# Performance work log

Hardware: AMD Instinct MI355X
Metric: run time of the kernel (lower is better)

## Reference

```python
import jax, jax.numpy as jnp
import numpy as np

B, C_IN, NF, H, W, L = 8, 64, 64, 96, 96, 13
NEG_SLOPE = 0.2


def conv2d(x, w, b, pad):
    # x: [B,C,H,W], w: [O,I,kh,kw]
    y = jax.lax.conv_general_dilated(
        x, w, window_strides=(1, 1), padding=[(pad, pad), (pad, pad)],
        dimension_numbers=("NCHW", "OIHW", "NCHW"))
    return y + b[None, :, None, None]


def leaky(x):
    return jax.nn.leaky_relu(x, NEG_SLOPE)


def bilinear_sample(img, px, py):
    # img: [B,C,H,W]; px,py: [B,H,W] pixel coords; zero padding outside.
    Bs, C, Hs, Ws = img.shape
    x0 = jnp.floor(px)
    y0 = jnp.floor(py)
    wx = px - x0
    wy = py - y0
    x0i = x0.astype(jnp.int32)
    y0i = y0.astype(jnp.int32)
    imgf = img.reshape(Bs, C, Hs * Ws)

    def gather(xi, yi):
        valid = ((xi >= 0) & (xi < Ws) & (yi >= 0) & (yi < Hs)).astype(img.dtype)
        xc = jnp.clip(xi, 0, Ws - 1)
        yc = jnp.clip(yi, 0, Hs - 1)
        idx = (yc * Ws + xc).reshape(Bs, 1, Hs * Ws)
        v = jnp.take_along_axis(imgf, idx, axis=2).reshape(Bs, C, Hs, Ws)
        return v * valid[:, None, :, :]

    return (gather(x0i, y0i) * ((1 - wx) * (1 - wy))[:, None]
            + gather(x0i + 1, y0i) * (wx * (1 - wy))[:, None]
            + gather(x0i, y0i + 1) * ((1 - wx) * wy)[:, None]
            + gather(x0i + 1, y0i + 1) * (wx * wy)[:, None])


def warp(img, flow):
    # img: [B,C,H,W]; flow: [B,2,H,W] (dx=flow[:,0], dy=flow[:,1])
    Bs, C, Hs, Ws = img.shape
    xx = jnp.arange(Ws, dtype=img.dtype)[None, None, :]  # [1,1,W]
    yy = jnp.arange(Hs, dtype=img.dtype)[None, :, None]  # [1,H,1]
    vx = xx + flow[:, 0]  # [B,H,W]
    vy = yy + flow[:, 1]
    # torch grid_sample(align_corners=False) with normalization 2*v/(dim-1)-1:
    # sample pixel = v*dim/(dim-1) - 0.5
    px = vx * (Ws / (Ws - 1)) - 0.5
    py = vy * (Hs / (Hs - 1)) - 0.5
    return bilinear_sample(img, px, py)


def setup_inputs() -> dict:
    key = jax.random.key(0)
    ks = jax.random.split(key, 13)
    s = 0.05
    return {
        "x": jax.random.normal(ks[0], (B, C_IN, H, W), jnp.float32),
        "m": jax.random.normal(ks[1], (B, NF, H, W), jnp.float32),
        "prev_h": jax.random.normal(ks[2], (B, NF, H, W), jnp.float32),
        "w_i2h": jax.random.normal(ks[3], (3 * NF, C_IN, 3, 3), jnp.float32) * s,
        "b_i2h": jnp.zeros((3 * NF,), jnp.float32),
        "w_i2f": jax.random.normal(ks[4], (32, C_IN, 5, 5), jnp.float32) * s,
        "b_i2f": jnp.zeros((32,), jnp.float32),
        "w_h2f": jax.random.normal(ks[5], (32, NF, 5, 5), jnp.float32) * s,
        "b_h2f": jnp.zeros((32,), jnp.float32),
        "w_fl": jax.random.normal(ks[6], (2 * L, 32, 5, 5), jnp.float32) * s,
        "b_fl": jnp.zeros((2 * L,), jnp.float32),
        "w_ret": jax.random.normal(ks[7], (3 * NF, NF * L, 1, 1), jnp.float32) * s,
        "b_ret": jnp.zeros((3 * NF,), jnp.float32),
    }


def reference(x, m, prev_h, w_i2h, b_i2h, w_i2f, b_i2f, w_h2f, b_h2f, w_fl, b_fl, w_ret, b_ret):
    # input-to-hidden gates
    i2h = conv2d(x, w_i2h, b_i2h, pad=1)              # [B,3NF,H,W]
    i0, i1, i2 = jnp.split(i2h, 3, axis=1)
    # flow generator
    f = leaky(conv2d(x, w_i2f, b_i2f, pad=2) + conv2d(prev_h, w_h2f, b_h2f, pad=2))
    flows = conv2d(f, w_fl, b_fl, pad=2)              # [B,2L,H,W]
    flows = flows.reshape(B, L, 2, H, W)
    # warp prev_h by -flow for each link (vectorized over L)
    warped = jax.vmap(lambda fl: warp(prev_h, -fl), in_axes=1, out_axes=1)(flows)
    warped = warped.reshape(B, L * NF, H, W)
    h2h = conv2d(warped, w_ret, b_ret, pad=0)         # [B,3NF,H,W]
    h0, h1, h2 = jnp.split(h2h, 3, axis=1)
    reset_gate = jax.nn.sigmoid(i0 + h0)
    update_gate = jax.nn.sigmoid(i1 + h1)
    new_mem = leaky(i2 + reset_gate * h2)
    next_h = update_gate * prev_h + (1.0 - update_gate) * new_mem
    return (next_h, m, next_h)
```

## Files before the change

kernel.cpp:

```cpp
#include <hip/hip_runtime.h>
#include <hip/hip_bf16.h>
#include <hip/hip_fp16.h>

typedef unsigned short u16;
typedef unsigned int u32;
typedef __attribute__((ext_vector_type(8))) _Float16 f16x8;
typedef __attribute__((ext_vector_type(4))) float f32x4;

#define NEG 0.2f

__device__ __forceinline__ float bf2f(u16 u) {
    return __uint_as_float(((u32)u) << 16);
}
__device__ __forceinline__ u16 f2b(float f) {
    u32 u = __float_as_uint(f);
    u32 r = (u + 0x7FFF + ((u >> 16) & 1)) >> 16;
    return (u16)r;
}
__device__ __forceinline__ u16 f2h(float f) {
    return __half_as_ushort(__float2half(f));
}
__device__ __forceinline__ float h2f(u16 u) {
    return __half2float(__ushort_as_half(u));
}
__device__ __forceinline__ float sigm(float x) {
    return 1.0f / (1.0f + __expf(-x));
}
__device__ __forceinline__ float ldin(const void* p, int idx, int flag) {
    if (flag) return ((const float*)p)[idx];
    return bf2f(((const u16*)p)[idx]);
}
__device__ __forceinline__ u16 ldin_h(const void* p, int idx, int flag) {
    if (flag) return f2h(((const float*)p)[idx]);
    return f2h(bf2f(((const u16*)p)[idx]));
}


#define WS_NEED 60371008u

__global__ void kdetect(const u16* __restrict__ x, u32* __restrict__ flag)
{
    __shared__ u32 mx[256];
    int t = threadIdx.x;
    u32 m = 0;
    for (int i = t; i < 8192; i += 256) {
        u32 e = ((u32)x[i] >> 7) & 0xFF;
        m = m > e ? m : e;
    }
    mx[t] = m;
    __syncthreads();
    for (int s = 128; s > 0; s >>= 1) {
        if (t < s) mx[t] = mx[t] > mx[t + s] ? mx[t] : mx[t + s];
        __syncthreads();
    }
    if (t == 0) flag[0] = (mx[0] > 0xC0) ? 1u : 0u;
}

__global__ void kprep(const void* __restrict__ w_i2h, const void* __restrict__ w_i2f,
                      const void* __restrict__ w_h2f, const void* __restrict__ w_fl,
                      const void* __restrict__ w_ret,
                      const void* __restrict__ b_i2h, const void* __restrict__ b_i2f,
                      const void* __restrict__ b_h2f, const void* __restrict__ b_fl,
                      const void* __restrict__ b_ret,
                      u16* __restrict__ wiA, u16* __restrict__ wfA,
                      u16* __restrict__ wlA, u16* __restrict__ wretA,
                      float* __restrict__ biases, const u32* __restrict__ flag)
{
    int flg = (int)flag[0];
    int i = blockIdx.x * 256 + threadIdx.x;
    if (i < 110592) {
        int j = i & 7; int lane = (i >> 3) & 63; int rest = i >> 9;
        int cib = rest & 1; int rest2 = rest >> 1;
        int tap = rest2 % 9; int mt = rest2 / 9;
        int oc = mt * 16 + (lane & 15);
        int ci = cib * 32 + ((lane >> 4) << 3) + j;
        wiA[i] = ldin_h(w_i2h, (oc * 64 + ci) * 9 + tap, flg);
    }
    if (i < 102400) {
        int j = i & 7; int lane = (i >> 3) & 63; int rest = i >> 9;
        int cib = rest & 3; int rest2 = rest >> 2;
        int tap = rest2 % 25; int mt = rest2 / 25;
        int oc = mt * 16 + (lane & 15);
        int cip = cib * 32 + ((lane >> 4) << 3) + j;
        wfA[i] = (cip < 64) ? ldin_h(w_i2f, (oc * 64 + cip) * 25 + tap, flg)
                            : ldin_h(w_h2f, (oc * 64 + cip - 64) * 25 + tap, flg);
    }
    if (i < 25600) {
        int j = i & 7; int lane = (i >> 3) & 63; int rest = i >> 9;
        int tap = rest % 25; int mt = rest / 25;
        int oc = mt * 16 + (lane & 15);
        int ci = ((lane >> 4) << 3) + j;
        wlA[i] = (oc < 26) ? ldin_h(w_fl, (oc * 32 + ci) * 25 + tap, flg) : (u16)0;
    }
    if (i < 159744) {
        int j = i & 7; int l = (i >> 3) & 63; int rest = i >> 9;
        int ks = rest % 26; int mt = rest / 26;
        int o = mt * 16 + (l & 15);
        int k = ks * 32 + ((l >> 4) << 3) + j;
        wretA[i] = ldin_h(w_ret, o * 832 + k, flg);
    }
    if (i < 474) {
        float v;
        if (i < 192)      v = ldin(b_i2h, i, flg);
        else if (i < 224) v = ldin(b_i2f, i - 192, flg);
        else if (i < 256) v = ldin(b_h2f, i - 224, flg);
        else if (i < 282) v = ldin(b_fl, i - 256, flg);
        else              v = ldin(b_ret, i - 282, flg);
        biases[i] = v;
    }
}

__global__ __launch_bounds__(256) void kxph(const void* __restrict__ x,
        const void* __restrict__ ph, u16* __restrict__ xph,
        const u32* __restrict__ flag)
{
    __shared__ __align__(16) u16 tile[64 * 104];
    int flg = (int)flag[0];
    int h = blockIdx.x, b = blockIdx.y;
    int t = threadIdx.x;
#pragma unroll 1
    for (int s = 0; s < 2; s++) {
        const void* src = s ? ph : x;
#pragma unroll 1
        for (int i = t; i < 768; i += 256) {
            int wc = i % 12, c = i / 12;
            int base = ((b * 64 + c) * 96 + h) * 96 + wc * 8;
            u16 r[8];
            if (flg) {
                const float* sp = (const float*)src + base;
                float4 f0 = *(const float4*)sp;
                float4 f1 = *(const float4*)(sp + 4);
                r[0] = f2h(f0.x); r[1] = f2h(f0.y); r[2] = f2h(f0.z); r[3] = f2h(f0.w);
                r[4] = f2h(f1.x); r[5] = f2h(f1.y); r[6] = f2h(f1.z); r[7] = f2h(f1.w);
            } else {
                const u16* sp = (const u16*)src + base;
                uint4 u = *(const uint4*)sp;
                r[0] = f2h(bf2f((u16)(u.x & 0xFFFF))); r[1] = f2h(bf2f((u16)(u.x >> 16)));
                r[2] = f2h(bf2f((u16)(u.y & 0xFFFF))); r[3] = f2h(bf2f((u16)(u.y >> 16)));
                r[4] = f2h(bf2f((u16)(u.z & 0xFFFF))); r[5] = f2h(bf2f((u16)(u.z >> 16)));
                r[6] = f2h(bf2f((u16)(u.w & 0xFFFF))); r[7] = f2h(bf2f((u16)(u.w >> 16)));
            }
            uint4 o;
            o.x = r[0] | ((u32)r[1] << 16); o.y = r[2] | ((u32)r[3] << 16);
            o.z = r[4] | ((u32)r[5] << 16); o.w = r[6] | ((u32)r[7] << 16);
            *(uint4*)&tile[c * 104 + wc * 8] = o;
        }
        __syncthreads();
#pragma unroll 1
        for (int i = t; i < 768; i += 256) {
            int cg = i & 7, w = i >> 3;
            u16 v[8];
#pragma unroll
            for (int k = 0; k < 8; k++) v[k] = tile[(cg * 8 + k) * 104 + w];
            uint4 o;
            o.x = v[0] | ((u32)v[1] << 16); o.y = v[2] | ((u32)v[3] << 16);
            o.z = v[4] | ((u32)v[5] << 16); o.w = v[6] | ((u32)v[7] << 16);
            *(uint4*)&xph[(((b * 96 + h) * 96 + w) << 7) + s * 64 + cg * 8] = o;
        }
        __syncthreads();
    }
}

__global__ __launch_bounds__(256) void k_i2h(const u16* __restrict__ xph,
        const u16* __restrict__ wiA, const float* __restrict__ biases,
        u16* __restrict__ i2hT)
{
    __shared__ __align__(16) u16 xl[3 * 98 * 72];
    int lin = blockIdx.x;
    int b = lin & 7;
    int h = lin >> 3;
    int t = threadIdx.x, lane = t & 63, wv = t >> 6;
    int n = lane & 15, quad = lane >> 4;

#pragma unroll 1
    for (int i = t; i < 2352; i += 256) {
        int co = i & 7; int pos = i >> 3; int xx = pos % 98; int yy = pos / 98;
        int gy = h + yy - 1, gx = xx - 1;
        uint4 v = make_uint4(0, 0, 0, 0);
        if (gy >= 0 && gy < 96 && gx >= 0 && gx < 96)
            v = *(const uint4*)&xph[((((b * 96 + gy) * 96 + gx)) << 7) + (co << 3)];
        *(uint4*)&xl[(yy * 98 + xx) * 72 + (co << 3)] = v;
    }
    __syncthreads();

    int mt0 = wv * 3;
    f32x4 acc[3][6] = {};
    const f16x8* A = (const f16x8*)wiA;
    f16x8 aC[3], aN[3];
#pragma unroll
    for (int mi = 0; mi < 3; mi++)
        aC[mi] = A[(((mt0 + mi) * 9 + 0) * 2 + 0) * 64 + lane];
#pragma unroll 1
    for (int it = 0; it < 18; it++) {
        int tap = it >> 1, cib = it & 1;
        if (it < 17) {
            int tn = it + 1; int tapn = tn >> 1, cibn = tn & 1;
#pragma unroll
            for (int mi = 0; mi < 3; mi++)
                aN[mi] = A[(((mt0 + mi) * 9 + tapn) * 2 + cibn) * 64 + lane];
        }
        int dy = tap / 3, dx = tap % 3;
        __builtin_amdgcn_s_setprio(1);
#pragma unroll
        for (int g = 0; g < 6; g++) {
            f16x8 bb = *(const f16x8*)&xl[(dy * 98 + g * 16 + n + dx) * 72 + cib * 32 + quad * 8];
#pragma unroll
            for (int mi = 0; mi < 3; mi++)
                acc[mi][g] = __builtin_amdgcn_mfma_f32_16x16x32_f16(aC[mi], bb, acc[mi][g], 0, 0, 0);
        }
        __builtin_amdgcn_s_setprio(0);
#pragma unroll
        for (int mi = 0; mi < 3; mi++) aC[mi] = aN[mi];
    }

#pragma unroll
    for (int mi = 0; mi < 3; mi++) {
        int ocb = (mt0 + mi) * 16 + quad * 4;
        float b0 = biases[ocb + 0], b1 = biases[ocb + 1];
        float b2 = biases[ocb + 2], b3 = biases[ocb + 3];
#pragma unroll
        for (int g = 0; g < 6; g++) {
            u16 p0 = f2h(acc[mi][g][0] + b0);
            u16 p1 = f2h(acc[mi][g][1] + b1);
            u16 p2 = f2h(acc[mi][g][2] + b2);
            u16 p3 = f2h(acc[mi][g][3] + b3);
            int base = (((b * 96 + h) * 96 + g * 16 + n)) * 192 + ocb;
            *(uint2*)&i2hT[base] =
                make_uint2(p0 | ((u32)p1 << 16), p2 | ((u32)p3 << 16));
        }
    }
}

__global__ __launch_bounds__(256) void k_flowfeat(const u16* __restrict__ xph,
        const u16* __restrict__ wfA, const float* __restrict__ biases,
        u16* __restrict__ fT)
{
    __shared__ __align__(16) u16 xl[8 * 20 * 136];
    int lin = blockIdx.x;
    int b = lin & 7;
    int r = lin >> 3;
    int x0 = (r % 6) * 16, y0 = (r / 6) * 4;
    int t = threadIdx.x, lane = t & 63, wv = t >> 6;
    int n = lane & 15, quad = lane >> 4;

    for (int i = t; i < 2560; i += 256) {
        int co = i & 15; int pos = i >> 4; int xx = pos % 20; int yy = pos / 20;
        int gy = y0 + yy - 2, gx = x0 + xx - 2;
        uint4 v = make_uint4(0, 0, 0, 0);
        if (gy >= 0 && gy < 96 && gx >= 0 && gx < 96)
            v = *(const uint4*)&xph[((((b * 96 + gy) * 96 + gx)) << 7) + (co << 3)];
        *(uint4*)&xl[(yy * 20 + xx) * 136 + (co << 3)] = v;
    }
    __syncthreads();

    f32x4 acc0 = {}, acc1 = {};
    const f16x8* A = (const f16x8*)wfA;
    f16x8 bbC[4], a0C[4], a1C[4];
    {
        int rowb = (wv * 20 + n) * 136 + quad * 8;
#pragma unroll
        for (int cib = 0; cib < 4; cib++) {
            bbC[cib] = *(const f16x8*)&xl[rowb + cib * 32];
            a0C[cib] = A[cib * 64 + lane];
            a1C[cib] = A[(100 + cib) * 64 + lane];
        }
    }
#pragma unroll 1
    for (int tap = 0; tap < 25; tap++) {
        f16x8 bbN[4], a0N[4], a1N[4];
        if (tap < 24) {
            int tn = tap + 1;
            int dy = tn / 5, dx = tn % 5;
            int rowb = ((wv + dy) * 20 + n + dx) * 136 + quad * 8;
#pragma unroll
            for (int cib = 0; cib < 4; cib++) {
                bbN[cib] = *(const f16x8*)&xl[rowb + cib * 32];
                a0N[cib] = A[(tn * 4 + cib) * 64 + lane];
                a1N[cib] = A[((25 + tn) * 4 + cib) * 64 + lane];
            }
        }
#pragma unroll
        for (int cib = 0; cib < 4; cib++) {
            acc0 = __builtin_amdgcn_mfma_f32_16x16x32_f16(a0C[cib], bbC[cib], acc0, 0, 0, 0);
            acc1 = __builtin_amdgcn_mfma_f32_16x16x32_f16(a1C[cib], bbC[cib], acc1, 0, 0, 0);
        }
#pragma unroll
        for (int cib = 0; cib < 4; cib++) {
            bbC[cib] = bbN[cib]; a0C[cib] = a0N[cib]; a1C[cib] = a1N[cib];
        }
    }

    int base = (((b * 96 + y0 + wv) * 96 + x0 + n)) * 32 + quad * 4;
    {
        u16 p[4];
#pragma unroll
        for (int r2 = 0; r2 < 4; r2++) {
            int oc = quad * 4 + r2;
            float v = acc0[r2] + biases[192 + oc] + biases[224 + oc];
            v = (v > 0.f) ? v : NEG * v;
            p[r2] = f2h(v);
        }
        *(uint2*)&fT[base] = make_uint2(p[0] | ((u32)p[1] << 16), p[2] | ((u32)p[3] << 16));
#pragma unroll
        for (int r2 = 0; r2 < 4; r2++) {
            int oc = 16 + quad * 4 + r2;
            float v = acc1[r2] + biases[192 + oc] + biases[224 + oc];
            v = (v > 0.f) ? v : NEG * v;
            p[r2] = f2h(v);
        }
        *(uint2*)&fT[base + 16] = make_uint2(p[0] | ((u32)p[1] << 16), p[2] | ((u32)p[3] << 16));
    }
}

__global__ __launch_bounds__(256) void k_flows(const u16* __restrict__ fT,
        const u16* __restrict__ wlA, const float* __restrict__ biases,
        float* __restrict__ flows)
{
    __shared__ __align__(16) u16 xl[8 * 20 * 40];
    int lin = blockIdx.x;
    int b = lin & 7;
    int r = lin >> 3;
    int x0 = (r % 6) * 16, y0 = (r / 6) * 4;
    int t = threadIdx.x, lane = t & 63, wv = t >> 6;
    int n = lane & 15, quad = lane >> 4;

    for (int i = t; i < 640; i += 256) {
        int co = i & 3; int pos = i >> 2; int xx = pos % 20; int yy = pos / 20;
        int gy = y0 + yy - 2, gx = x0 + xx - 2;
        uint4 v = make_uint4(0, 0, 0, 0);
        if (gy >= 0 && gy < 96 && gx >= 0 && gx < 96)
            v = *(const uint4*)&fT[((((b * 96 + gy) * 96 + gx)) << 5) + (co << 3)];
        *(uint4*)&xl[(yy * 20 + xx) * 40 + (co << 3)] = v;
    }
    __syncthreads();

    f32x4 acc0 = {}, acc1 = {};
    const f16x8* A = (const f16x8*)wlA;
#pragma unroll 5
    for (int tap = 0; tap < 25; tap++) {
        int dy = tap / 5, dx = tap % 5;
        f16x8 bb = *(const f16x8*)&xl[((wv + dy) * 20 + n + dx) * 40 + quad * 8];
        f16x8 a0 = A[tap * 64 + lane];
        f16x8 a1 = A[(25 + tap) * 64 + lane];
        acc0 = __builtin_amdgcn_mfma_f32_16x16x32_f16(a0, bb, acc0, 0, 0, 0);
        acc1 = __builtin_amdgcn_mfma_f32_16x16x32_f16(a1, bb, acc1, 0, 0, 0);
    }

    int pix = (y0 + wv) * 96 + x0 + n;
#pragma unroll
    for (int r2 = 0; r2 < 4; r2++) {
        int oc = quad * 4 + r2;
        flows[(b * 26 + oc) * 9216 + pix] = acc0[r2] + biases[256 + oc];
        int oc1 = 16 + quad * 4 + r2;
        if (oc1 < 26)
            flows[(b * 26 + oc1) * 9216 + pix] = acc1[r2] + biases[256 + oc1];
    }
}

__global__ __launch_bounds__(256, 4) void k_fused(const float* __restrict__ flows,
        const u16* __restrict__ xph, const u16* __restrict__ i2hT,
        const u16* __restrict__ wretA, const float* __restrict__ biases,
        void* __restrict__ out, const u32* __restrict__ flag)
{
    __shared__ __align__(16) u16 gb[2][32][72];
    __shared__ __align__(16) float hh[192 * 33];

    int flg = (int)flag[0];
    int lin = blockIdx.x;
    int b = lin & 7;
    int r = lin >> 3;
    int w0 = (r % 3) * 32;
    int h = r / 3;
    int t = threadIdx.x;
    int lane = t & 63, wv = t >> 6;
    const float S = 96.f / 95.f;
    int hrow = h * 96 + w0;

    int p = t >> 3, sub = t & 7;
    const float* fl = &flows[b * 26 * 9216 + hrow + p];
    const u16* xb = &xph[(b * 96) * 96 * 128 + 64 + sub * 8];

    int n = lane & 15, q = lane >> 4;
    int mt0 = wv * 3;
    f32x4 acc[3][2] = {};
    const f16x8* Ap = (const f16x8*)wretA;
    const f16x8 zv = {};

    f16x8 c00, c10, c01, c11; float cwx, cwy;
    f16x8 n00, n10, n01, n11; float nwx, nwy;
    float fdxc, fdyc, fdxn, fdyn;

#define GISSUE(DX, DY, V00, V10, V01, V11, WX, WY)                         \
    {                                                                      \
        float px = ((float)(w0 + p) - (DX)) * S - 0.5f;                    \
        float py = ((float)h - (DY)) * S - 0.5f;                           \
        float fx = floorf(px), fy = floorf(py);                            \
        int ix = (int)fx, iy = (int)fy;                                    \
        WX = px - fx; WY = py - fy;                                        \
        bool xv0 = (ix >= 0) & (ix < 96);                                  \
        bool xv1 = (ix >= -1) & (ix < 95);                                 \
        bool yv0 = (iy >= 0) & (iy < 96);                                  \
        bool yv1 = (iy >= -1) & (iy < 95);                                 \
        V00 = zv; V10 = zv; V01 = zv; V11 = zv;                            \
        if (yv0) {                                                         \
            const u16* rr = xb + (iy * 96 + ix) * 128;                     \
            if (xv0) V00 = *(const f16x8*)rr;                              \
            if (xv1) V10 = *(const f16x8*)(rr + 128);                      \
        }                                                                  \
        if (yv1) {                                                         \
            const u16* rr = xb + ((iy + 1) * 96 + ix) * 128;               \
            if (xv0) V01 = *(const f16x8*)rr;                              \
            if (xv1) V11 = *(const f16x8*)(rr + 128);                      \
        }                                                                  \
    }

    fdxc = fl[0 * 9216]; fdyc = fl[1 * 9216];
    fdxn = fl[2 * 9216]; fdyn = fl[3 * 9216];
    GISSUE(fdxc, fdyc, c00, c10, c01, c11, cwx, cwy);

#pragma unroll
    for (int l = 0; l < 13; l++) {
        float fdx2 = 0.f, fdy2 = 0.f;
        if (l + 2 < 13) { fdx2 = fl[(2 * l + 4) * 9216]; fdy2 = fl[(2 * l + 5) * 9216]; }
        if (l + 1 < 13) GISSUE(fdxn, fdyn, n00, n10, n01, n11, nwx, nwy);
        {
            float w00 = (1.f - cwx) * (1.f - cwy), w10 = cwx * (1.f - cwy);
            float w01 = (1.f - cwx) * cwy,         w11 = cwx * cwy;
            u16 res[8];
#pragma unroll
            for (int j = 0; j < 8; j++) {
                float v = w00 * (float)c00[j] + w10 * (float)c10[j]
                        + w01 * (float)c01[j] + w11 * (float)c11[j];
                res[j] = f2h(v);
            }
            uint4 o;
            o.x = res[0] | ((u32)res[1] << 16); o.y = res[2] | ((u32)res[3] << 16);
            o.z = res[4] | ((u32)res[5] << 16); o.w = res[6] | ((u32)res[7] << 16);
            *(uint4*)&gb[l & 1][p][sub * 8] = o;
        }
        __syncthreads();
        __builtin_amdgcn_s_setprio(1);
#pragma unroll
        for (int ksl = 0; ksl < 2; ksl++) {
            int ks = 2 * l + ksl;
            f16x8 b0 = *(const f16x8*)&gb[l & 1][n][ksl * 32 + q * 8];
            f16x8 b1 = *(const f16x8*)&gb[l & 1][16 + n][ksl * 32 + q * 8];
#pragma unroll
            for (int mi = 0; mi < 3; mi++) {
                f16x8 a = Ap[((mt0 + mi) * 26 + ks) * 64 + lane];
                acc[mi][0] = __builtin_amdgcn_mfma_f32_16x16x32_f16(a, b0, acc[mi][0], 0, 0, 0);
                acc[mi][1] = __builtin_amdgcn_mfma_f32_16x16x32_f16(a, b1, acc[mi][1], 0, 0, 0);
            }
        }
        __builtin_amdgcn_s_setprio(0);
        c00 = n00; c10 = n10; c01 = n01; c11 = n11; cwx = nwx; cwy = nwy;
        fdxc = fdxn; fdyc = fdyn; fdxn = fdx2; fdyn = fdy2;
    }
#undef GISSUE

#pragma unroll
    for (int mi = 0; mi < 3; mi++) {
        int ob = (mt0 + mi) * 16 + q * 4;
#pragma unroll
        for (int ni = 0; ni < 2; ni++)
#pragma unroll
            for (int r2 = 0; r2 < 4; r2++) {
                int o = ob + r2;
                hh[o * 33 + ni * 16 + n] = acc[mi][ni][r2] + biases[282 + o];
            }
    }
    __syncthreads();

#pragma unroll 1
    for (int j = 0; j < 8; j++) {
        int i = t + 256 * j;
        int cc = i & 63, pp = i >> 6;
        float h0v = hh[cc * 33 + pp];
        float h1v = hh[(64 + cc) * 33 + pp];
        float h2v = hh[(128 + cc) * 33 + pp];
        int pix = (b * 96 + h) * 96 + w0 + pp;
        float i0 = h2f(i2hT[pix * 192 + cc]);
        float i1 = h2f(i2hT[pix * 192 + 64 + cc]);
        float i2 = h2f(i2hT[pix * 192 + 128 + cc]);
        float pv = h2f(xph[(pix << 7) + 64 + cc]);
        float rg = sigm(i0 + h0v);
        float ug = sigm(i1 + h1v);
        float nm = i2 + rg * h2v;
        nm = (nm > 0.f) ? nm : NEG * nm;
        float nh = ug * pv + (1.f - ug) * nm;
        hh[cc * 33 + pp] = nh;
    }
    __syncthreads();

#pragma unroll 1
    for (int j = 0; j < 8; j++) {
        int i = t + 256 * j;
        int pp = i & 31, cc = i >> 5;
        float nh = hh[cc * 33 + pp];
        int oidx = ((b * 64 + cc) * 96 + h) * 96 + w0 + pp;
        if (flg) {
            float* of = (float*)out;
            of[oidx] = nh;
            of[oidx + 2 * 4718592] = nh;
        } else {
            u16* ob16 = (u16*)out;
            u16 v = f2b(nh);
            ob16[oidx] = v;
            ob16[oidx + 2 * 4718592] = v;
        }
    }
}

__global__ void kcopym(const uint4* __restrict__ m, uint4* __restrict__ out,
                       const u32* __restrict__ flag)
{
    int flg = (int)flag[0];
    int n4 = flg ? 1179648 : 589824;
    int stride = gridDim.x * 256;
    for (int i = blockIdx.x * 256 + threadIdx.x; i < n4; i += stride)
        out[n4 + i] = m[i];
}

extern "C" void kernel_launch(void* const* d_in, const int* in_sizes, int n_in,
                              void* d_out, int out_size, void* d_ws, size_t ws_size,
                              hipStream_t stream)
{
    const void* x     = d_in[0];
    const void* m     = d_in[1];
    const void* ph    = d_in[2];
    const void* w_i2h = d_in[3];
    const void* b_i2h = d_in[4];
    const void* w_i2f = d_in[5];
    const void* b_i2f = d_in[6];
    const void* w_h2f = d_in[7];
    const void* b_h2f = d_in[8];
    const void* w_fl  = d_in[9];
    const void* b_fl  = d_in[10];
    const void* w_ret = d_in[11];
    const void* b_ret = d_in[12];

    char* ws = (char*)d_ws;
    u32*    flag   = (u32*)  (ws + 0);
    u16*    wiA    = (u16*)  (ws + 64);
    u16*    wfA    = (u16*)  (ws + 221248);
    u16*    wlA    = (u16*)  (ws + 426048);
    u16*    wretA  = (u16*)  (ws + 477248);
    float*  biases = (float*)(ws + 796736);
    u16*    xph    = (u16*)  (ws + 798784);
    u16*    i2hT   = (u16*)  (ws + 19673152);
    u16*    fT     = (u16*)  (ws + 47984704);
    float*  flows  = (float*)(ws + 52703296);
    if (ws_size < WS_NEED) return;

    kdetect<<<1, 256, 0, stream>>>((const u16*)x, flag);
    kprep<<<624, 256, 0, stream>>>(w_i2h, w_i2f, w_h2f, w_fl, w_ret,
                                   b_i2h, b_i2f, b_h2f, b_fl, b_ret,
                                   wiA, wfA, wlA, wretA, biases, flag);
    kxph<<<dim3(96, 8), 256, 0, stream>>>(x, ph, xph, flag);
    k_i2h<<<dim3(768), 256, 0, stream>>>(xph, wiA, biases, i2hT);
    k_flowfeat<<<dim3(1152), 256, 0, stream>>>(xph, wfA, biases, fT);
    k_flows<<<dim3(1152), 256, 0, stream>>>(fT, wlA, biases, flows);
    k_fused<<<dim3(2304), 256, 0, stream>>>(flows, xph, i2hT, wretA, biases,
                                            d_out, flag);
    kcopym<<<2048, 256, 0, stream>>>((const uint4*)m, (uint4*)d_out, flag);
}
```

Before: 293.0 us.

## Fuse i2h convolution into the fused warp/GRU kernel and drop the i2hT buffer

Removes the separate k_i2h kernel and computes the 3x3 input-to-hidden convolution inside k_fused, staging a 3-row x tile with an XOR-swizzled layout in shared memory. The output-channel-to-wave mapping changes to wv+4*mi so that each thread holds matching i0/i1/i2 and h0/h1/h2 values, which lets the GRU gate math run directly on registers instead of through a 192-channel shared-memory staging pass. This cuts the i2hT global write and read traffic and one kernel launch, and shrinks shared memory. In exchange, k_fused gains more registers and extra prologue work while launch bounds ask for 4 blocks per CU.

```diff
diff --git a/kernel.cpp b/kernel.cpp
--- a/kernel.cpp
+++ b/kernel.cpp
@@ -161,76 +161,6 @@
     }
 }
 
-__global__ __launch_bounds__(256) void k_i2h(const u16* __restrict__ xph,
-        const u16* __restrict__ wiA, const float* __restrict__ biases,
-        u16* __restrict__ i2hT)
-{
-    __shared__ __align__(16) u16 xl[3 * 98 * 72];
-    int lin = blockIdx.x;
-    int b = lin & 7;
-    int h = lin >> 3;
-    int t = threadIdx.x, lane = t & 63, wv = t >> 6;
-    int n = lane & 15, quad = lane >> 4;
-
-#pragma unroll 1
-    for (int i = t; i < 2352; i += 256) {
-        int co = i & 7; int pos = i >> 3; int xx = pos % 98; int yy = pos / 98;
-        int gy = h + yy - 1, gx = xx - 1;
-        uint4 v = make_uint4(0, 0, 0, 0);
-        if (gy >= 0 && gy < 96 && gx >= 0 && gx < 96)
-            v = *(const uint4*)&xph[((((b * 96 + gy) * 96 + gx)) << 7) + (co << 3)];
-        *(uint4*)&xl[(yy * 98 + xx) * 72 + (co << 3)] = v;
-    }
-    __syncthreads();
-
-    int mt0 = wv * 3;
-    f32x4 acc[3][6] = {};
-    const f16x8* A = (const f16x8*)wiA;
-    f16x8 aC[3], aN[3];
-#pragma unroll
-    for (int mi = 0; mi < 3; mi++)
-        aC[mi] = A[(((mt0 + mi) * 9 + 0) * 2 + 0) * 64 + lane];
-#pragma unroll 1
-    for (int it = 0; it < 18; it++) {
-        int tap = it >> 1, cib = it & 1;
-        if (it < 17) {
-            int tn = it + 1; int tapn = tn >> 1, cibn = tn & 1;
-#pragma unroll
-            for (int mi = 0; mi < 3; mi++)
-                aN[mi] = A[(((mt0 + mi) * 9 + tapn) * 2 + cibn) * 64 + lane];
-        }
-        int dy = tap / 3, dx = tap % 3;
-        __builtin_amdgcn_s_setprio(1);
-#pragma unroll
-        for (int g = 0; g < 6; g++) {
-            f16x8 bb = *(const f16x8*)&xl[(dy * 98 + g * 16 + n + dx) * 72 + cib * 32 + quad * 8];
-#pragma unroll
-            for (int mi = 0; mi < 3; mi++)
-                acc[mi][g] = __builtin_amdgcn_mfma_f32_16x16x32_f16(aC[mi], bb, acc[mi][g], 0, 0, 0);
-        }
-        __builtin_amdgcn_s_setprio(0);
-#pragma unroll
-        for (int mi = 0; mi < 3; mi++) aC[mi] = aN[mi];
-    }
-
-#pragma unroll
-    for (int mi = 0; mi < 3; mi++) {
-        int ocb = (mt0 + mi) * 16 + quad * 4;
-        float b0 = biases[ocb + 0], b1 = biases[ocb + 1];
-        float b2 = biases[ocb + 2], b3 = biases[ocb + 3];
-#pragma unroll
-        for (int g = 0; g < 6; g++) {
-            u16 p0 = f2h(acc[mi][g][0] + b0);
-            u16 p1 = f2h(acc[mi][g][1] + b1);
-            u16 p2 = f2h(acc[mi][g][2] + b2);
-            u16 p3 = f2h(acc[mi][g][3] + b3);
-            int base = (((b * 96 + h) * 96 + g * 16 + n)) * 192 + ocb;
-            *(uint2*)&i2hT[base] =
-                make_uint2(p0 | ((u32)p1 << 16), p2 | ((u32)p3 << 16));
-        }
-    }
-}
-
 __global__ __launch_bounds__(256) void k_flowfeat(const u16* __restrict__ xph,
         const u16* __restrict__ wfA, const float* __restrict__ biases,
         u16* __restrict__ fT)
@@ -358,12 +288,15 @@
 }
 
 __global__ __launch_bounds__(256, 4) void k_fused(const float* __restrict__ flows,
-        const u16* __restrict__ xph, const u16* __restrict__ i2hT,
+        const u16* __restrict__ xph, const u16* __restrict__ wiA,
         const u16* __restrict__ wretA, const float* __restrict__ biases,
         void* __restrict__ out, const u32* __restrict__ flag)
 {
-    __shared__ __align__(16) u16 gb[2][32][72];
-    __shared__ __align__(16) float hh[192 * 33];
+    __shared__ __align__(16) char sm[26368];
+    u16* xi  = (u16*)sm;
+    u16* pvs = (u16*)(sm + 13056);
+    u16 (*gb)[32][72] = (u16 (*)[32][72])(sm + 17152);
+    float* wst = (float*)(sm + 17152);
 
     int flg = (int)flag[0];
     int lin = blockIdx.x;
@@ -376,27 +309,78 @@
     const float S = 96.f / 95.f;
     int hrow = h * 96 + w0;
 
+#pragma unroll 1
+    for (int i = t; i < 816; i += 256) {
+        int co = i & 7; int pos = i >> 3;
+        int px = pos % 34, dy = pos / 34;
+        int gy = h + dy - 1, gx = w0 + px - 1;
+        uint4 v = make_uint4(0, 0, 0, 0);
+        if (gy >= 0 && gy < 96 && gx >= 0 && gx < 96)
+            v = *(const uint4*)&xph[(((b * 96 + gy) * 96 + gx) << 7) + (co << 3)];
+        *(uint4*)&xi[((dy * 34 + px) << 6) + ((co ^ (px & 7)) << 3)] = v;
+    }
+    {
+        int co = t & 7; int px = t >> 3;
+        uint4 v = *(const uint4*)&xph[(((b * 96 + h) * 96 + w0 + px) << 7) + 64 + (co << 3)];
+        *(uint4*)&pvs[(px << 6) + ((co ^ (px & 7)) << 3)] = v;
+    }
+    __syncthreads();
+
     int p = t >> 3, sub = t & 7;
     const float* fl = &flows[b * 26 * 9216 + hrow + p];
     const u16* xb = &xph[(b * 96) * 96 * 128 + 64 + sub * 8];
 
     int n = lane & 15, q = lane >> 4;
-    int mt0 = wv * 3;
+    const f16x8* Ap = (const f16x8*)wretA;
+    const f16x8* Ai = (const f16x8*)wiA;
+    const f16x8 zv = {};
+
+    float fdxc = fl[0 * 9216], fdyc = fl[1 * 9216];
+    float fdxn = fl[2 * 9216], fdyn = fl[3 * 9216];
+
+    f32x4 acc2[3][2] = {};
+    {
+        f16x8 aC[3], aN[3];
+#pragma unroll
+        for (int mi = 0; mi < 3; mi++)
+            aC[mi] = Ai[(((wv + 4 * mi) * 9 + 0) * 2 + 0) * 64 + lane];
+#pragma unroll 1
+        for (int it = 0; it < 18; it++) {
+            int tap = it >> 1, cib = it & 1;
+            if (it < 17) {
+                int tn = it + 1; int tapn = tn >> 1, cibn = tn & 1;
+#pragma unroll
+                for (int mi = 0; mi < 3; mi++)
+                    aN[mi] = Ai[(((wv + 4 * mi) * 9 + tapn) * 2 + cibn) * 64 + lane];
+            }
+            int dy = tap / 3, dx = tap % 3;
+            __builtin_amdgcn_s_setprio(1);
+#pragma unroll
+            for (int g = 0; g < 2; g++) {
+                int px = g * 16 + n + dx;
+                int cor = (cib * 4 + q) ^ (px & 7);
+                f16x8 bb = *(const f16x8*)&xi[((dy * 34 + px) << 6) + (cor << 3)];
+#pragma unroll
+                for (int mi = 0; mi < 3; mi++)
+                    acc2[mi][g] = __builtin_amdgcn_mfma_f32_16x16x32_f16(aC[mi], bb, acc2[mi][g], 0, 0, 0);
+            }
+            __builtin_amdgcn_s_setprio(0);
+#pragma unroll
+            for (int mi = 0; mi < 3; mi++) aC[mi] = aN[mi];
+        }
+    }
+
     f32x4 acc[3][2] = {};
-    const f16x8* Ap = (const f16x8*)wretA;
-    const f16x8 zv = {};
-
     f16x8 c00, c10, c01, c11; float cwx, cwy;
     f16x8 n00, n10, n01, n11; float nwx, nwy;
-    float fdxc, fdyc, fdxn, fdyn;
 
 #define GISSUE(DX, DY, V00, V10, V01, V11, WX, WY)                         \
     {                                                                      \
-        float px = ((float)(w0 + p) - (DX)) * S - 0.5f;                    \
-        float py = ((float)h - (DY)) * S - 0.5f;                           \
-        float fx = floorf(px), fy = floorf(py);                            \
+        float px_ = ((float)(w0 + p) - (DX)) * S - 0.5f;                   \
+        float py_ = ((float)h - (DY)) * S - 0.5f;                          \
+        float fx = floorf(px_), fy = floorf(py_);                          \
         int ix = (int)fx, iy = (int)fy;                                    \
-        WX = px - fx; WY = py - fy;                                        \
+        WX = px_ - fx; WY = py_ - fy;                                      \
         bool xv0 = (ix >= 0) & (ix < 96);                                  \
         bool xv1 = (ix >= -1) & (ix < 95);                                 \
         bool yv0 = (iy >= 0) & (iy < 96);                                  \
@@ -414,8 +398,6 @@
         }                                                                  \
     }
 
-    fdxc = fl[0 * 9216]; fdyc = fl[1 * 9216];
-    fdxn = fl[2 * 9216]; fdyn = fl[3 * 9216];
     GISSUE(fdxc, fdyc, c00, c10, c01, c11, cwx, cwy);
 
 #pragma unroll
@@ -447,7 +429,7 @@
             f16x8 b1 = *(const f16x8*)&gb[l & 1][16 + n][ksl * 32 + q * 8];
 #pragma unroll
             for (int mi = 0; mi < 3; mi++) {
-                f16x8 a = Ap[((mt0 + mi) * 26 + ks) * 64 + lane];
+                f16x8 a = Ap[((wv + 4 * mi) * 26 + ks) * 64 + lane];
                 acc[mi][0] = __builtin_amdgcn_mfma_f32_16x16x32_f16(a, b0, acc[mi][0], 0, 0, 0);
                 acc[mi][1] = __builtin_amdgcn_mfma_f32_16x16x32_f16(a, b1, acc[mi][1], 0, 0, 0);
             }
@@ -458,45 +440,35 @@
     }
 #undef GISSUE
 
-#pragma unroll
-    for (int mi = 0; mi < 3; mi++) {
-        int ob = (mt0 + mi) * 16 + q * 4;
-#pragma unroll
-        for (int ni = 0; ni < 2; ni++)
-#pragma unroll
-            for (int r2 = 0; r2 < 4; r2++) {
-                int o = ob + r2;
-                hh[o * 33 + ni * 16 + n] = acc[mi][ni][r2] + biases[282 + o];
-            }
-    }
     __syncthreads();
 
-#pragma unroll 1
-    for (int j = 0; j < 8; j++) {
-        int i = t + 256 * j;
-        int cc = i & 63, pp = i >> 6;
-        float h0v = hh[cc * 33 + pp];
-        float h1v = hh[(64 + cc) * 33 + pp];
-        float h2v = hh[(128 + cc) * 33 + pp];
-        int pix = (b * 96 + h) * 96 + w0 + pp;
-        float i0 = h2f(i2hT[pix * 192 + cc]);
-        float i1 = h2f(i2hT[pix * 192 + 64 + cc]);
-        float i2 = h2f(i2hT[pix * 192 + 128 + cc]);
-        float pv = h2f(xph[(pix << 7) + 64 + cc]);
-        float rg = sigm(i0 + h0v);
-        float ug = sigm(i1 + h1v);
-        float nm = i2 + rg * h2v;
-        nm = (nm > 0.f) ? nm : NEG * nm;
-        float nh = ug * pv + (1.f - ug) * nm;
-        hh[cc * 33 + pp] = nh;
-    }
+#pragma unroll
+    for (int ni = 0; ni < 2; ni++)
+#pragma unroll
+        for (int r2 = 0; r2 < 4; r2++) {
+            int ocg = wv * 16 + q * 4 + r2;
+            int px = ni * 16 + n;
+            float i0 = acc2[0][ni][r2] + biases[ocg];
+            float i1 = acc2[1][ni][r2] + biases[64 + ocg];
+            float i2 = acc2[2][ni][r2] + biases[128 + ocg];
+            float h0 = acc[0][ni][r2] + biases[282 + ocg];
+            float h1 = acc[1][ni][r2] + biases[282 + 64 + ocg];
+            float h2 = acc[2][ni][r2] + biases[282 + 128 + ocg];
+            int cor = (ocg >> 3) ^ (px & 7);
+            float pv = h2f(pvs[(px << 6) + (cor << 3) + (ocg & 7)]);
+            float rg = sigm(i0 + h0);
+            float ug = sigm(i1 + h1);
+            float nm = i2 + rg * h2;
+            nm = (nm > 0.f) ? nm : NEG * nm;
+            wst[ocg * 32 + px] = ug * pv + (1.f - ug) * nm;
+        }
     __syncthreads();
 
 #pragma unroll 1
     for (int j = 0; j < 8; j++) {
         int i = t + 256 * j;
         int pp = i & 31, cc = i >> 5;
-        float nh = hh[cc * 33 + pp];
+        float nh = wst[cc * 32 + pp];
         int oidx = ((b * 64 + cc) * 96 + h) * 96 + w0 + pp;
         if (flg) {
             float* of = (float*)out;
@@ -547,7 +519,6 @@
     u16*    wretA  = (u16*)  (ws + 477248);
     float*  biases = (float*)(ws + 796736);
     u16*    xph    = (u16*)  (ws + 798784);
-    u16*    i2hT   = (u16*)  (ws + 19673152);
     u16*    fT     = (u16*)  (ws + 47984704);
     float*  flows  = (float*)(ws + 52703296);
     if (ws_size < WS_NEED) return;
@@ -557,10 +528,9 @@
                                    b_i2h, b_i2f, b_h2f, b_fl, b_ret,
                                    wiA, wfA, wlA, wretA, biases, flag);
     kxph<<<dim3(96, 8), 256, 0, stream>>>(x, ph, xph, flag);
-    k_i2h<<<dim3(768), 256, 0, stream>>>(xph, wiA, biases, i2hT);
     k_flowfeat<<<dim3(1152), 256, 0, stream>>>(xph, wfA, biases, fT);
     k_flows<<<dim3(1152), 256, 0, stream>>>(fT, wlA, biases, flows);
-    k_fused<<<dim3(2304), 256, 0, stream>>>(flows, xph, i2hT, wretA, biases,
+    k_fused<<<dim3(2304), 256, 0, stream>>>(flows, xph, wiA, wretA, biases,
                                             d_out, flag);
     kcopym<<<2048, 256, 0, stream>>>((const uint4*)m, (uint4*)d_out, flag);
 }
```

New measurement: 283.7 us. -3.2%, faster.
